# Optimization experiments

Hardware: AMD Instinct MI355X
Metric: run time of the kernel (lower is better)

The kernel has to match this reference:

```python
import jax, jax.numpy as jnp
import numpy as np

B, L, DIN, DQK = 16, 1024, 512, 128
NL, NC = 2, 2  # number of 'learnable' heads, number of 'cnn_projection' heads


def _conv1d(x_bcl, w, b):
    # x: [B, C_in, L], w: [C_out, C_in, 3], 'same' padding (kernel 3 -> pad 1)
    y = jax.lax.conv_general_dilated(x_bcl, w, (1,), [(1, 1)],
                                     dimension_numbers=('NCH', 'OIH', 'NCH'))
    return y + b[None, :, None]


def _attend(q, k, v, scale):
    # q,k,v: [H, B, L, D]; scale: [H]
    inv = 1.0 / jnp.sqrt(jnp.asarray(q.shape[-1], q.dtype))
    att = jax.nn.softmax(jnp.einsum('hbld,hbmd->hblm', q, k) * inv, axis=-1)
    out = scale[:, None, None, None] * jnp.einsum('hblm,hbmd->hbld', att, v)
    return out, att


def setup_inputs() -> dict:
    rk = jax.random.key(0)
    ks = jax.random.split(rk, 24)
    s = 0.02
    d = {}
    d['query'] = jax.random.normal(ks[0], (B, L, DIN), jnp.float32)
    d['key']   = jax.random.normal(ks[1], (B, L, DIN), jnp.float32)
    d['value'] = jax.random.normal(ks[2], (B, L, DIN), jnp.float32)
    # learnable (KQVProduct) heads: Linear dim_in -> dim_qk, stored as [in,out]
    d['lw_q'] = jax.random.normal(ks[3], (NL, DIN, DQK), jnp.float32) * s
    d['lb_q'] = jnp.zeros((NL, DQK), jnp.float32)
    d['lw_k'] = jax.random.normal(ks[4], (NL, DIN, DQK), jnp.float32) * s
    d['lb_k'] = jnp.zeros((NL, DQK), jnp.float32)
    d['lw_v'] = jax.random.normal(ks[5], (NL, DIN, DQK), jnp.float32) * s
    d['lb_v'] = jnp.zeros((NL, DQK), jnp.float32)
    d['lscale'] = jnp.ones((NL,), jnp.float32)
    # cnn_projection (KQVPCNN) heads: Conv1d(dim_in, dim_qk, k=3, pad=1)
    d['cw_q'] = jax.random.normal(ks[6], (NC, DQK, DIN, 3), jnp.float32) * s
    d['cb_q'] = jnp.zeros((NC, DQK), jnp.float32)
    d['cw_k'] = jax.random.normal(ks[7], (NC, DQK, DIN, 3), jnp.float32) * s
    d['cb_k'] = jnp.zeros((NC, DQK), jnp.float32)
    d['cw_v'] = jax.random.normal(ks[8], (NC, DQK, DIN, 3), jnp.float32) * s
    d['cb_v'] = jnp.zeros((NC, DQK), jnp.float32)
    d['cscale'] = jnp.ones((NC,), jnp.float32)
    # final projection: Linear((NL+NC)*dim_qk -> dim_in)
    d['proj_w'] = jax.random.normal(ks[9], ((NL + NC) * DQK, DIN), jnp.float32) * s
    d['proj_b'] = jnp.zeros((DIN,), jnp.float32)
    return d


def reference(query, key, value,
              lw_q, lb_q, lw_k, lb_k, lw_v, lb_v, lscale,
              cw_q, cb_q, cw_k, cb_k, cw_v, cb_v, cscale,
              proj_w, proj_b):
    # --- learnable heads (batched over head axis) ---
    lq = jnp.einsum('bld,hdk->hblk', query, lw_q) + lb_q[:, None, None, :]
    lk = jnp.einsum('bld,hdk->hblk', key,   lw_k) + lb_k[:, None, None, :]
    lv = jnp.einsum('bld,hdk->hblk', value, lw_v) + lb_v[:, None, None, :]
    lout, latt = _attend(lq, lk, lv, lscale)
    # --- cnn_projection heads ---
    qt = jnp.swapaxes(query, 1, 2)  # [B, DIN, L]
    kt = jnp.swapaxes(key, 1, 2)
    vt = jnp.swapaxes(value, 1, 2)
    cq = jnp.swapaxes(jax.vmap(lambda w, b: _conv1d(qt, w, b))(cw_q, cb_q), 2, 3)
    ck = jnp.swapaxes(jax.vmap(lambda w, b: _conv1d(kt, w, b))(cw_k, cb_k), 2, 3)
    cv = jnp.swapaxes(jax.vmap(lambda w, b: _conv1d(vt, w, b))(cw_v, cb_v), 2, 3)
    cout, catt = _attend(cq, ck, cv, cscale)  # [NC, B, L, DQK]
    # --- concat heads + final projection ---
    cat = jnp.concatenate([lout[0], lout[1], cout[0], cout[1]], axis=-1)  # [B,L,4*DQK]
    out = cat @ proj_w + proj_b
    return (out, latt[0], latt[1], catt[0], catt[1])
```

## Files before the change

### kernel.cpp

```cpp
#include <hip/hip_runtime.h>


using bf16_t = __bf16;
using bf16x8 = __attribute__((ext_vector_type(8))) __bf16;
using bf16x4 = __attribute__((ext_vector_type(4))) __bf16;
using f32x4  = __attribute__((ext_vector_type(4))) float;

#define NB   16
#define SL   1024
#define DIN  512
#define DQK  128
#define NH   4

#define BK 32

constexpr size_t XPAD_ROWS  = (size_t)NB * (SL + 2);
constexpr size_t XPAD_PER   = XPAD_ROWS * DIN;
constexpr size_t XPAD_ELEMS = 3 * XPAD_PER;
constexpr size_t WT_ELEMS   = (size_t)3 * NH * 3 * DQK * DIN;
constexpr size_t PWT_ELEMS  = (size_t)DIN * DIN;
constexpr size_t BIAS_ELEMS = (size_t)3 * NH * DQK;
constexpr size_t QH_ELEMS   = (size_t)NH * NB * SL * DQK;
constexpr size_t PART_ELEMS = (size_t)NH * NB * 8 * SL;
constexpr size_t CAT_ELEMS  = (size_t)NB * SL * (NH * DQK);

#define INV_SQRT_DK 0.08838834764831845f

__device__ __forceinline__ void load_lds_16B(const void* g, void* l) {
  __builtin_amdgcn_global_load_lds((const __attribute__((address_space(1))) void*)g,
                                   (__attribute__((address_space(3))) void*)l, 16, 0, 0);
}

__device__ __forceinline__ void gemm_core(const bf16_t* __restrict__ Ab, int lda,
                                          const bf16_t* __restrict__ Bb, int ldb,
                                          int K, f32x4 acc[4][4],
                                          bf16_t* lgA, bf16_t* lgB) {
  const int tid  = threadIdx.x;
  const int wave = tid >> 6;
  const int lane = tid & 63;
  const int quad = lane >> 4;
  const int l16  = lane & 15;
  const int wr   = wave >> 1;
  const int wc   = wave & 1;
  const int lrow = lane >> 2;
  const int lcol = (lane & 3) << 3;

  for (int k0 = 0; k0 < K; k0 += BK) {
    __syncthreads();
#pragma unroll
    for (int c = 0; c < 2; ++c) {
      const int chunk = wave * 2 + c;
      const int r = chunk * 16 + lrow;
      load_lds_16B(Ab + (size_t)r * lda + k0 + lcol, lgA + chunk * 512);
      load_lds_16B(Bb + (size_t)r * ldb + k0 + lcol, lgB + chunk * 512);
    }
    __syncthreads();
    bf16x8 af[4], bfr[4];
#pragma unroll
    for (int i = 0; i < 4; ++i)
      af[i] = *(const bf16x8*)(lgA + (wr * 64 + i * 16 + l16) * BK + quad * 8);
#pragma unroll
    for (int i = 0; i < 4; ++i)
      bfr[i] = *(const bf16x8*)(lgB + (wc * 64 + i * 16 + l16) * BK + quad * 8);
#pragma unroll
    for (int mi = 0; mi < 4; ++mi)
#pragma unroll
      for (int ni = 0; ni < 4; ++ni)
        acc[mi][ni] = __builtin_amdgcn_mfma_f32_16x16x32_bf16(af[mi], bfr[ni],
                                                              acc[mi][ni], 0, 0, 0);
  }
}

#define GEMM_PROLOGUE()                                    \
  __shared__ __align__(16) bf16_t lgA[128 * BK];           \
  __shared__ __align__(16) bf16_t lgB[128 * BK];           \
  f32x4 acc[4][4];                                         \
  {                                                        \
    f32x4 z = {0.f, 0.f, 0.f, 0.f};                        \
    _Pragma("unroll") for (int i = 0; i < 4; ++i)          \
      _Pragma("unroll") for (int j = 0; j < 4; ++j)        \
        acc[i][j] = z;                                     \
  }

#define EPILOGUE_VARS()                                    \
  const int wave = threadIdx.x >> 6;                       \
  const int lane = threadIdx.x & 63;                       \
  const int quad = lane >> 4;                              \
  const int l16  = lane & 15;                              \
  const int wr   = wave >> 1;                              \
  const int wc   = wave & 1;


__global__ void cast_pad_kernel(const float* __restrict__ q,
                                const float* __restrict__ k,
                                const float* __restrict__ v,
                                bf16_t* __restrict__ xpad) {
  size_t i = (size_t)blockIdx.x * blockDim.x + threadIdx.x;
  if (i >= XPAD_ELEMS / 8) return;
  int    s    = (int)(i / (XPAD_PER / 8));
  size_t r    = i % (XPAD_PER / 8);
  size_t rowg = r >> 6;
  int    c0   = (int)(r & 63) * 8;
  size_t b    = rowg / (SL + 2);
  int    row  = (int)(rowg % (SL + 2));
  const float* src = (s == 0) ? q : ((s == 1) ? k : v);
  bf16x8 o;
  if (row == 0 || row == SL + 1) {
#pragma unroll
    for (int j = 0; j < 8; ++j) o[j] = (bf16_t)0.f;
  } else {
    const float* p = src + ((b * SL) + row - 1) * DIN + c0;
    const float4 f0 = ((const float4*)p)[0];
    const float4 f1 = ((const float4*)p)[1];
    o[0] = (bf16_t)f0.x; o[1] = (bf16_t)f0.y; o[2] = (bf16_t)f0.z; o[3] = (bf16_t)f0.w;
    o[4] = (bf16_t)f1.x; o[5] = (bf16_t)f1.y; o[6] = (bf16_t)f1.z; o[7] = (bf16_t)f1.w;
  }
  *(bf16x8*)(xpad + i * 8) = o;
}

__global__ void prep_w_kernel(const float* __restrict__ lw_q, const float* __restrict__ lw_k,
                              const float* __restrict__ lw_v, const float* __restrict__ lb_q,
                              const float* __restrict__ lb_k, const float* __restrict__ lb_v,
                              const float* __restrict__ cw_q, const float* __restrict__ cw_k,
                              const float* __restrict__ cw_v, const float* __restrict__ cb_q,
                              const float* __restrict__ cb_k, const float* __restrict__ cb_v,
                              const float* __restrict__ proj_w,
                              bf16_t* __restrict__ Wt, float* __restrict__ bias,
                              bf16_t* __restrict__ pwt) {
  size_t i = (size_t)blockIdx.x * blockDim.x + threadIdx.x;
  if (i < WT_ELEMS) {
    int kk = (int)(i % DIN);
    int n  = (int)((i / DIN) % DQK);
    int t  = (int)((i / ((size_t)DIN * DQK)) % 3);
    int h  = (int)((i / ((size_t)DIN * DQK * 3)) % NH);
    int s  = (int)(i / ((size_t)DIN * DQK * 3 * NH));
    const float* lw = (s == 0) ? lw_q : ((s == 1) ? lw_k : lw_v);
    const float* cw = (s == 0) ? cw_q : ((s == 1) ? cw_k : cw_v);
    float val;
    if (h < 2) val = (t == 1) ? lw[((size_t)h * DIN + kk) * DQK + n] : 0.f;
    else       val = cw[(((size_t)(h - 2) * DQK + n) * DIN + kk) * 3 + t];
    Wt[i] = (bf16_t)val;
  } else if (i < WT_ELEMS + PWT_ELEMS) {
    size_t j = i - WT_ELEMS;
    int n = (int)(j / DIN), kk = (int)(j % DIN);
    pwt[j] = (bf16_t)proj_w[(size_t)kk * DIN + n];
  } else if (i < WT_ELEMS + PWT_ELEMS + BIAS_ELEMS) {
    size_t j = i - WT_ELEMS - PWT_ELEMS;
    int s = (int)(j / (NH * DQK));
    int h = (int)((j / DQK) % NH);
    int n = (int)(j % DQK);
    const float* lb = (s == 0) ? lb_q : ((s == 1) ? lb_k : lb_v);
    const float* cb = (s == 0) ? cb_q : ((s == 1) ? cb_k : cb_v);
    bias[j] = (h < 2) ? lb[h * DQK + n] : cb[(h - 2) * DQK + n];
  }
}

__global__ __launch_bounds__(256, 2) void proj_kernel(
    const bf16_t* __restrict__ xpad, const bf16_t* __restrict__ Wt,
    const float* __restrict__ bias,
    bf16_t* __restrict__ Qh, bf16_t* __restrict__ Kh, bf16_t* __restrict__ Vt) {
  GEMM_PROLOGUE();
  const int mt = blockIdx.x;
  const int z  = blockIdx.z;
  const int s  = z >> 2, h = (z & 3) ^ 2;
  const int b  = mt >> 3;
  const int l0 = (mt & 7) << 7;

  const bf16_t* Xs = xpad + (size_t)s * XPAD_PER;
  const int t0 = (h < 2) ? 1 : 0;
  const int t1 = (h < 2) ? 1 : 2;
  for (int t = t0; t <= t1; ++t) {
    const bf16_t* Ab = Xs + ((size_t)b * (SL + 2) + l0 + t) * DIN;
    const bf16_t* Bb = Wt + (((size_t)(s * NH + h) * 3 + t) * DQK) * DIN;
    gemm_core(Ab, DIN, Bb, DIN, DIN, acc, lgA, lgB);
  }

  EPILOGUE_VARS();
  const float* bs = bias + (s * NH + h) * DQK;
  if (s < 2) {
    bf16_t* outp = ((s == 0) ? Qh : Kh) + ((size_t)h * NB + b) * SL * DQK
                 + (size_t)l0 * DQK;
#pragma unroll
    for (int mi = 0; mi < 4; ++mi)
#pragma unroll
      for (int ni = 0; ni < 4; ++ni)
#pragma unroll
        for (int r = 0; r < 4; ++r) {
          int row = wr * 64 + mi * 16 + quad * 4 + r;
          int col = wc * 64 + ni * 16 + l16;
          outp[(size_t)row * DQK + col] = (bf16_t)(acc[mi][ni][r] + bs[col]);
        }
  } else {
    bf16_t* outv = Vt + ((size_t)h * NB + b) * DQK * SL;
#pragma unroll
    for (int mi = 0; mi < 4; ++mi)
#pragma unroll
      for (int ni = 0; ni < 4; ++ni)
#pragma unroll
        for (int r = 0; r < 4; ++r) {
          int row = wr * 64 + mi * 16 + quad * 4 + r;
          int col = wc * 64 + ni * 16 + l16;
          outv[(size_t)col * SL + l0 + row] = (bf16_t)(acc[mi][ni][r] + bs[col]);
        }
  }
}

__global__ __launch_bounds__(256, 2) void sgemm_kernel(
    const bf16_t* __restrict__ Qh, const bf16_t* __restrict__ Kh,
    float* __restrict__ att, float2* __restrict__ partials) {
  GEMM_PROLOGUE();
  const int mt = blockIdx.x;
  const int nt = blockIdx.y;
  const int hb = blockIdx.z;
  const bf16_t* Ab = Qh + (size_t)hb * SL * DQK + (size_t)mt * 128 * DQK;
  const bf16_t* Bb = Kh + (size_t)hb * SL * DQK + (size_t)nt * 128 * DQK;
  gemm_core(Ab, DQK, Bb, DQK, DQK, acc, lgA, lgB);

  EPILOGUE_VARS();
  const int tid = threadIdx.x;
#pragma unroll
  for (int mi = 0; mi < 4; ++mi)
#pragma unroll
    for (int ni = 0; ni < 4; ++ni)
#pragma unroll
      for (int r = 0; r < 4; ++r)
        acc[mi][ni][r] *= INV_SQRT_DK;

  float* outp = att + (size_t)hb * SL * SL;
#pragma unroll
  for (int mi = 0; mi < 4; ++mi)
#pragma unroll
    for (int ni = 0; ni < 4; ++ni)
#pragma unroll
      for (int r = 0; r < 4; ++r) {
        int row = mt * 128 + wr * 64 + mi * 16 + quad * 4 + r;
        int col = nt * 128 + wc * 64 + ni * 16 + l16;
        outp[(size_t)row * SL + col] = acc[mi][ni][r];
      }

  __syncthreads();
  float* smM = (float*)lgA;
  float* smS = smM + 256;
#pragma unroll
  for (int mi = 0; mi < 4; ++mi)
#pragma unroll
    for (int r = 0; r < 4; ++r) {
      float m = acc[mi][0][r];
#pragma unroll
      for (int ni = 1; ni < 4; ++ni) m = fmaxf(m, acc[mi][ni][r]);
      m = fmaxf(m, __shfl_xor(m, 1, 64));
      m = fmaxf(m, __shfl_xor(m, 2, 64));
      m = fmaxf(m, __shfl_xor(m, 4, 64));
      m = fmaxf(m, __shfl_xor(m, 8, 64));
      float s = 0.f;
#pragma unroll
      for (int ni = 0; ni < 4; ++ni) s += __expf(acc[mi][ni][r] - m);
      s += __shfl_xor(s, 1, 64);
      s += __shfl_xor(s, 2, 64);
      s += __shfl_xor(s, 4, 64);
      s += __shfl_xor(s, 8, 64);
      if (l16 == 0) {
        int row = wr * 64 + mi * 16 + quad * 4 + r;
        smM[row * 2 + wc] = m;
        smS[row * 2 + wc] = s;
      }
    }
  __syncthreads();
  if (tid < 128) {
    float m0 = smM[tid * 2], m1 = smM[tid * 2 + 1];
    float s0 = smS[tid * 2], s1 = smS[tid * 2 + 1];
    float m = fmaxf(m0, m1);
    float s = s0 * __expf(m0 - m) + s1 * __expf(m1 - m);
    partials[((size_t)hb * 8 + nt) * SL + (size_t)mt * 128 + tid] =
        make_float2(m, s);
  }
}

__global__ __launch_bounds__(256, 2) void av_kernel(
    float* __restrict__ att, const float2* __restrict__ partials,
    const bf16_t* __restrict__ Vt,
    const float* __restrict__ lscale, const float* __restrict__ cscale,
    bf16_t* __restrict__ cat) {
  __shared__ __align__(16) bf16_t lgA[128 * BK];
  __shared__ __align__(16) bf16_t lgB[128 * BK];
  __shared__ float rowM[128];
  __shared__ float rowInv[128];
  f32x4 acc[4][4];
  {
    f32x4 z = {0.f, 0.f, 0.f, 0.f};
#pragma unroll
    for (int i = 0; i < 4; ++i)
#pragma unroll
      for (int j = 0; j < 4; ++j) acc[i][j] = z;
  }
  const int mt = blockIdx.x;
  const int hb = blockIdx.z;
  const int h = hb >> 4, b = hb & 15;
  const int tid = threadIdx.x;

  if (tid < 128) {
    const size_t g = (size_t)mt * 128 + tid;
    float2 t[8];
    float m = -__builtin_inff();
#pragma unroll
    for (int nt = 0; nt < 8; ++nt) {
      t[nt] = partials[((size_t)hb * 8 + nt) * SL + g];
      m = fmaxf(m, t[nt].x);
    }
    float s = 0.f;
#pragma unroll
    for (int nt = 0; nt < 8; ++nt) s += t[nt].y * __expf(t[nt].x - m);
    rowM[tid] = m;
    rowInv[tid] = 1.0f / s;
  }
  __syncthreads();

  const int arow = tid >> 1;
  const int acol = (tid & 1) * 16;
  const float rm = rowM[arow];
  const float ri = rowInv[arow];
  float* Sp = att + (size_t)hb * SL * SL + ((size_t)mt * 128 + arow) * SL + acol;

  const int wave = tid >> 6;
  const int lane = tid & 63;
  const int quad = lane >> 4;
  const int l16  = lane & 15;
  const int wr   = wave >> 1;
  const int wc   = wave & 1;
  const int lrow = lane >> 2;
  const int lcol = (lane & 3) << 3;
  const bf16_t* Bb = Vt + (size_t)hb * DQK * SL;

  float4 f0 = ((const float4*)Sp)[0];
  float4 f1 = ((const float4*)Sp)[1];
  float4 f2 = ((const float4*)Sp)[2];
  float4 f3 = ((const float4*)Sp)[3];

  for (int k0 = 0; k0 < SL; k0 += BK) {
    __syncthreads();
    float4 p0, p1, p2, p3;
    p0.x = __expf(f0.x - rm) * ri; p0.y = __expf(f0.y - rm) * ri;
    p0.z = __expf(f0.z - rm) * ri; p0.w = __expf(f0.w - rm) * ri;
    p1.x = __expf(f1.x - rm) * ri; p1.y = __expf(f1.y - rm) * ri;
    p1.z = __expf(f1.z - rm) * ri; p1.w = __expf(f1.w - rm) * ri;
    p2.x = __expf(f2.x - rm) * ri; p2.y = __expf(f2.y - rm) * ri;
    p2.z = __expf(f2.z - rm) * ri; p2.w = __expf(f2.w - rm) * ri;
    p3.x = __expf(f3.x - rm) * ri; p3.y = __expf(f3.y - rm) * ri;
    p3.z = __expf(f3.z - rm) * ri; p3.w = __expf(f3.w - rm) * ri;
    ((float4*)(Sp + k0))[0] = p0;
    ((float4*)(Sp + k0))[1] = p1;
    ((float4*)(Sp + k0))[2] = p2;
    ((float4*)(Sp + k0))[3] = p3;
    bf16x8 o0 = {(bf16_t)p0.x, (bf16_t)p0.y, (bf16_t)p0.z, (bf16_t)p0.w,
                 (bf16_t)p1.x, (bf16_t)p1.y, (bf16_t)p1.z, (bf16_t)p1.w};
    bf16x8 o1 = {(bf16_t)p2.x, (bf16_t)p2.y, (bf16_t)p2.z, (bf16_t)p2.w,
                 (bf16_t)p3.x, (bf16_t)p3.y, (bf16_t)p3.z, (bf16_t)p3.w};
    *(bf16x8*)(lgA + arow * BK + acol)     = o0;
    *(bf16x8*)(lgA + arow * BK + acol + 8) = o1;
    if (k0 + BK < SL) {
      f0 = ((const float4*)(Sp + k0 + BK))[0];
      f1 = ((const float4*)(Sp + k0 + BK))[1];
      f2 = ((const float4*)(Sp + k0 + BK))[2];
      f3 = ((const float4*)(Sp + k0 + BK))[3];
    }
#pragma unroll
    for (int c = 0; c < 2; ++c) {
      const int chunk = wave * 2 + c;
      const int r = chunk * 16 + lrow;
      load_lds_16B(Bb + (size_t)r * SL + k0 + lcol, lgB + chunk * 512);
    }
    __syncthreads();
    bf16x8 af[4], bfr[4];
#pragma unroll
    for (int i = 0; i < 4; ++i)
      af[i] = *(const bf16x8*)(lgA + (wr * 64 + i * 16 + l16) * BK + quad * 8);
#pragma unroll
    for (int i = 0; i < 4; ++i)
      bfr[i] = *(const bf16x8*)(lgB + (wc * 64 + i * 16 + l16) * BK + quad * 8);
#pragma unroll
    for (int mi = 0; mi < 4; ++mi)
#pragma unroll
      for (int ni = 0; ni < 4; ++ni)
        acc[mi][ni] = __builtin_amdgcn_mfma_f32_16x16x32_bf16(af[mi], bfr[ni],
                                                              acc[mi][ni], 0, 0, 0);
  }

  const float sc = (h < 2) ? lscale[h] : cscale[h - 2];
  bf16_t* outp = cat + (size_t)b * SL * (NH * DQK) + (size_t)(mt * 128) * (NH * DQK)
               + h * DQK;
#pragma unroll
  for (int mi = 0; mi < 4; ++mi)
#pragma unroll
    for (int ni = 0; ni < 4; ++ni)
#pragma unroll
      for (int r = 0; r < 4; ++r) {
        int row = wr * 64 + mi * 16 + quad * 4 + r;
        int col = wc * 64 + ni * 16 + l16;
        outp[(size_t)row * (NH * DQK) + col] = (bf16_t)(acc[mi][ni][r] * sc);
      }
}

__global__ __launch_bounds__(256, 2) void final_kernel(
    const bf16_t* __restrict__ cat, const bf16_t* __restrict__ pwt,
    const float* __restrict__ pb, float* __restrict__ outp) {
  GEMM_PROLOGUE();
  const int mt = blockIdx.x;
  const int nt = blockIdx.y;
  const bf16_t* Ab = cat + (size_t)mt * 128 * DIN;
  const bf16_t* Bb = pwt + (size_t)nt * 128 * DIN;
  gemm_core(Ab, DIN, Bb, DIN, DIN, acc, lgA, lgB);

  EPILOGUE_VARS();
#pragma unroll
  for (int mi = 0; mi < 4; ++mi)
#pragma unroll
    for (int ni = 0; ni < 4; ++ni)
#pragma unroll
      for (int r = 0; r < 4; ++r) {
        int row = mt * 128 + wr * 64 + mi * 16 + quad * 4 + r;
        int col = nt * 128 + wc * 64 + ni * 16 + l16;
        outp[(size_t)row * DIN + col] = acc[mi][ni][r] + pb[nt * 128 + col];
      }
}


extern "C" void kernel_launch(void* const* d_in, const int* in_sizes, int n_in,
                              void* d_out, int out_size, void* d_ws, size_t ws_size,
                              hipStream_t stream) {
  const float* q      = (const float*)d_in[0];
  const float* k      = (const float*)d_in[1];
  const float* v      = (const float*)d_in[2];
  const float* lw_q   = (const float*)d_in[3];
  const float* lb_q   = (const float*)d_in[4];
  const float* lw_k   = (const float*)d_in[5];
  const float* lb_k   = (const float*)d_in[6];
  const float* lw_v   = (const float*)d_in[7];
  const float* lb_v   = (const float*)d_in[8];
  const float* lscale = (const float*)d_in[9];
  const float* cw_q   = (const float*)d_in[10];
  const float* cb_q   = (const float*)d_in[11];
  const float* cw_k   = (const float*)d_in[12];
  const float* cb_k   = (const float*)d_in[13];
  const float* cw_v   = (const float*)d_in[14];
  const float* cb_v   = (const float*)d_in[15];
  const float* cscale = (const float*)d_in[16];
  const float* proj_w = (const float*)d_in[17];
  const float* proj_b = (const float*)d_in[18];

  char* ws = (char*)d_ws;
  size_t off = 0;
  bf16_t* xpad  = (bf16_t*)(ws + off); off += XPAD_ELEMS * 2;
  bf16_t* Wt    = (bf16_t*)(ws + off); off += WT_ELEMS * 2;
  float*  bias  = (float*) (ws + off); off += BIAS_ELEMS * 4;
  bf16_t* pwt   = (bf16_t*)(ws + off); off += PWT_ELEMS * 2;
  bf16_t* Qh    = (bf16_t*)(ws + off); off += QH_ELEMS * 2;
  bf16_t* Kh    = (bf16_t*)(ws + off); off += QH_ELEMS * 2;
  bf16_t* Vt    = (bf16_t*)(ws + off); off += QH_ELEMS * 2;
  float2* parts = (float2*)(ws + off); off += PART_ELEMS * 8;
  bf16_t* cat   = (bf16_t*)(ws + off); off += CAT_ELEMS * 2;

  float* outp = (float*)d_out;
  float* att  = outp + (size_t)NB * SL * DIN;

  {
    int nblk = (int)((XPAD_ELEMS / 8 + 255) / 256);
    cast_pad_kernel<<<nblk, 256, 0, stream>>>(q, k, v, xpad);
  }
  {
    size_t tot = WT_ELEMS + PWT_ELEMS + BIAS_ELEMS;
    int nblk = (int)((tot + 255) / 256);
    prep_w_kernel<<<nblk, 256, 0, stream>>>(lw_q, lw_k, lw_v, lb_q, lb_k, lb_v,
                                            cw_q, cw_k, cw_v, cb_q, cb_k, cb_v,
                                            proj_w, Wt, bias, pwt);
  }
  proj_kernel<<<dim3(128, 1, 12), 256, 0, stream>>>(xpad, Wt, bias, Qh, Kh, Vt);
  sgemm_kernel<<<dim3(8, 8, 64), 256, 0, stream>>>(Qh, Kh, att, parts);
  av_kernel<<<dim3(8, 1, 64), 256, 0, stream>>>(att, parts, Vt, lscale, cscale, cat);
  final_kernel<<<dim3(128, 4, 1), 256, 0, stream>>>(cat, pwt, proj_b, outp);
}
```

Before: 680.9 us.

## Store local exponentials in score kernel and rescale per 64-column chunk

The score GEMM epilogue now writes exp(s - local_max) for each 64-column half-tile instead of raw scaled scores. It also stores per-chunk (max, sum) partials directly, which drops the LDS reduction and its two barriers. The AV kernel builds a per-row, per-chunk correction factor once, so its inner loop does one multiply per element instead of an exp. This moves transcendental work out of the inner loop, at the cost of a larger partials buffer and 16-way combination per row.

```diff
diff --git a/kernel.cpp b/kernel.cpp
--- a/kernel.cpp
+++ b/kernel.cpp
@@ -21,7 +21,7 @@
 constexpr size_t PWT_ELEMS  = (size_t)DIN * DIN;
 constexpr size_t BIAS_ELEMS = (size_t)3 * NH * DQK;
 constexpr size_t QH_ELEMS   = (size_t)NH * NB * SL * DQK;
-constexpr size_t PART_ELEMS = (size_t)NH * NB * 8 * SL;
+constexpr size_t PART_ELEMS = (size_t)NH * NB * SL * 16;
 constexpr size_t CAT_ELEMS  = (size_t)NB * SL * (NH * DQK);
 
 #define INV_SQRT_DK 0.08838834764831845f
@@ -217,63 +217,36 @@
   gemm_core(Ab, DQK, Bb, DQK, DQK, acc, lgA, lgB);
 
   EPILOGUE_VARS();
-  const int tid = threadIdx.x;
+  float*  outp = att + (size_t)hb * SL * SL;
+  float2* pp   = partials + (size_t)hb * SL * 16;
 #pragma unroll
   for (int mi = 0; mi < 4; ++mi)
 #pragma unroll
-    for (int ni = 0; ni < 4; ++ni)
-#pragma unroll
-      for (int r = 0; r < 4; ++r)
-        acc[mi][ni][r] *= INV_SQRT_DK;
-
-  float* outp = att + (size_t)hb * SL * SL;
-#pragma unroll
-  for (int mi = 0; mi < 4; ++mi)
-#pragma unroll
-    for (int ni = 0; ni < 4; ++ni)
-#pragma unroll
-      for (int r = 0; r < 4; ++r) {
-        int row = mt * 128 + wr * 64 + mi * 16 + quad * 4 + r;
-        int col = nt * 128 + wc * 64 + ni * 16 + l16;
-        outp[(size_t)row * SL + col] = acc[mi][ni][r];
-      }
-
-  __syncthreads();
-  float* smM = (float*)lgA;
-  float* smS = smM + 256;
-#pragma unroll
-  for (int mi = 0; mi < 4; ++mi)
-#pragma unroll
     for (int r = 0; r < 4; ++r) {
-      float m = acc[mi][0][r];
-#pragma unroll
-      for (int ni = 1; ni < 4; ++ni) m = fmaxf(m, acc[mi][ni][r]);
+      float vv[4];
+#pragma unroll
+      for (int ni = 0; ni < 4; ++ni) vv[ni] = acc[mi][ni][r] * INV_SQRT_DK;
+      float m = fmaxf(fmaxf(vv[0], vv[1]), fmaxf(vv[2], vv[3]));
       m = fmaxf(m, __shfl_xor(m, 1, 64));
       m = fmaxf(m, __shfl_xor(m, 2, 64));
       m = fmaxf(m, __shfl_xor(m, 4, 64));
       m = fmaxf(m, __shfl_xor(m, 8, 64));
+      const int row = mt * 128 + wr * 64 + mi * 16 + quad * 4 + r;
       float s = 0.f;
 #pragma unroll
-      for (int ni = 0; ni < 4; ++ni) s += __expf(acc[mi][ni][r] - m);
+      for (int ni = 0; ni < 4; ++ni) {
+        float e = __expf(vv[ni] - m);
+        s += e;
+        int col = nt * 128 + wc * 64 + ni * 16 + l16;
+        outp[(size_t)row * SL + col] = e;
+      }
       s += __shfl_xor(s, 1, 64);
       s += __shfl_xor(s, 2, 64);
       s += __shfl_xor(s, 4, 64);
       s += __shfl_xor(s, 8, 64);
-      if (l16 == 0) {
-        int row = wr * 64 + mi * 16 + quad * 4 + r;
-        smM[row * 2 + wc] = m;
-        smS[row * 2 + wc] = s;
-      }
+      if (l16 == 0)
+        pp[(size_t)row * 16 + nt * 2 + wc] = make_float2(m, s);
     }
-  __syncthreads();
-  if (tid < 128) {
-    float m0 = smM[tid * 2], m1 = smM[tid * 2 + 1];
-    float s0 = smS[tid * 2], s1 = smS[tid * 2 + 1];
-    float m = fmaxf(m0, m1);
-    float s = s0 * __expf(m0 - m) + s1 * __expf(m1 - m);
-    partials[((size_t)hb * 8 + nt) * SL + (size_t)mt * 128 + tid] =
-        make_float2(m, s);
-  }
 }
 
 __global__ __launch_bounds__(256, 2) void av_kernel(
@@ -283,8 +256,7 @@
     bf16_t* __restrict__ cat) {
   __shared__ __align__(16) bf16_t lgA[128 * BK];
   __shared__ __align__(16) bf16_t lgB[128 * BK];
-  __shared__ float rowM[128];
-  __shared__ float rowInv[128];
+  __shared__ float cf[128][17];
   f32x4 acc[4][4];
   {
     f32x4 z = {0.f, 0.f, 0.f, 0.f};
@@ -299,26 +271,25 @@
   const int tid = threadIdx.x;
 
   if (tid < 128) {
-    const size_t g = (size_t)mt * 128 + tid;
-    float2 t[8];
+    const float2* pp = partials + ((size_t)hb * SL + (size_t)mt * 128 + tid) * 16;
+    float2 t[16];
     float m = -__builtin_inff();
 #pragma unroll
-    for (int nt = 0; nt < 8; ++nt) {
-      t[nt] = partials[((size_t)hb * 8 + nt) * SL + g];
-      m = fmaxf(m, t[nt].x);
+    for (int i = 0; i < 16; ++i) {
+      t[i] = pp[i];
+      m = fmaxf(m, t[i].x);
     }
     float s = 0.f;
 #pragma unroll
-    for (int nt = 0; nt < 8; ++nt) s += t[nt].y * __expf(t[nt].x - m);
-    rowM[tid] = m;
-    rowInv[tid] = 1.0f / s;
+    for (int i = 0; i < 16; ++i) s += t[i].y * __expf(t[i].x - m);
+    const float inv = 1.0f / s;
+#pragma unroll
+    for (int i = 0; i < 16; ++i) cf[tid][i] = __expf(t[i].x - m) * inv;
   }
   __syncthreads();
 
   const int arow = tid >> 1;
   const int acol = (tid & 1) * 16;
-  const float rm = rowM[arow];
-  const float ri = rowInv[arow];
   float* Sp = att + (size_t)hb * SL * SL + ((size_t)mt * 128 + arow) * SL + acol;
 
   const int wave = tid >> 6;
@@ -338,15 +309,12 @@
 
   for (int k0 = 0; k0 < SL; k0 += BK) {
     __syncthreads();
+    const float c = cf[arow][k0 >> 6];
     float4 p0, p1, p2, p3;
-    p0.x = __expf(f0.x - rm) * ri; p0.y = __expf(f0.y - rm) * ri;
-    p0.z = __expf(f0.z - rm) * ri; p0.w = __expf(f0.w - rm) * ri;
-    p1.x = __expf(f1.x - rm) * ri; p1.y = __expf(f1.y - rm) * ri;
-    p1.z = __expf(f1.z - rm) * ri; p1.w = __expf(f1.w - rm) * ri;
-    p2.x = __expf(f2.x - rm) * ri; p2.y = __expf(f2.y - rm) * ri;
-    p2.z = __expf(f2.z - rm) * ri; p2.w = __expf(f2.w - rm) * ri;
-    p3.x = __expf(f3.x - rm) * ri; p3.y = __expf(f3.y - rm) * ri;
-    p3.z = __expf(f3.z - rm) * ri; p3.w = __expf(f3.w - rm) * ri;
+    p0.x = f0.x * c; p0.y = f0.y * c; p0.z = f0.z * c; p0.w = f0.w * c;
+    p1.x = f1.x * c; p1.y = f1.y * c; p1.z = f1.z * c; p1.w = f1.w * c;
+    p2.x = f2.x * c; p2.y = f2.y * c; p2.z = f2.z * c; p2.w = f2.w * c;
+    p3.x = f3.x * c; p3.y = f3.y * c; p3.z = f3.z * c; p3.w = f3.w * c;
     ((float4*)(Sp + k0))[0] = p0;
     ((float4*)(Sp + k0))[1] = p1;
     ((float4*)(Sp + k0))[2] = p2;
@@ -364,8 +332,8 @@
       f3 = ((const float4*)(Sp + k0 + BK))[3];
     }
 #pragma unroll
-    for (int c = 0; c < 2; ++c) {
-      const int chunk = wave * 2 + c;
+    for (int c2 = 0; c2 < 2; ++c2) {
+      const int chunk = wave * 2 + c2;
       const int r = chunk * 16 + lrow;
       load_lds_16B(Bb + (size_t)r * SL + k0 + lcol, lgB + chunk * 512);
     }
```

After: 687.4 us. No clear change (+1.0%).
